# Kernel optimization log

Hardware: AMD Instinct MI355X
Metric: run time of the kernel (lower is better)

## Reference

```python
import jax, jax.numpy as jnp
import numpy as np

B, S, H, R = 32, 1024, 1024, 53
EPS = 1e-12
ATT_EPS = 1e10


def setup_inputs() -> dict:
    key = jax.random.key(0)
    ks = jax.random.split(key, 20)
    sc = 0.02
    n = lambda k, shape: jax.random.normal(k, shape, jnp.float32) * sc
    return {
        "relation": jax.random.randint(ks[0], (B, 1), 0, R),
        "last_hidden_size": jax.random.normal(ks[1], (B, S, H), jnp.float32),
        "sub_head": jax.random.randint(ks[2], (B, 1), 0, S),
        "sub_tail": jax.random.randint(ks[3], (B, 1), 0, S),
        "attention_mask": jax.random.randint(ks[4], (B, S), 0, 2).astype(jnp.int32),
        # learned params
        "rel_emb": n(ks[5], (R, H)),
        "Wrf": n(ks[6], (H, H)), "brf": jnp.zeros((H,), jnp.float32),
        "cln_w": jnp.ones((H,), jnp.float32), "cln_b": jnp.zeros((H,), jnp.float32),
        "Wwd": n(ks[7], (H, 2 * H)), "Wbd": n(ks[8], (H, 2 * H)),
        "Wq": n(ks[9], (H, H)), "bq": jnp.zeros((H,), jnp.float32),
        "Wk": n(ks[10], (H, H)), "bk": jnp.zeros((H,), jnp.float32),
        "Wv": n(ks[11], (H, H)), "bv": jnp.zeros((H,), jnp.float32),
        "Wo": n(ks[12], (1, H)), "bo": jnp.zeros((1,), jnp.float32),
    }


def reference(relation, last_hidden_size, sub_head, sub_tail, attention_mask,
              rel_emb, Wrf, brf, cln_w, cln_b, Wwd, Wbd,
              Wq, bq, Wk, bk, Wv, bv, Wo, bo):
    x = last_hidden_size  # [B,S,H]; dropout is identity at inference
    # relation feature: embedding -> linear -> ReLU6
    rel = jnp.clip(jnp.einsum('boh,gh->bog', rel_emb[relation], Wrf) + brf, 0.0, 6.0)  # [B,1,H]
    # gather subject head/tail token features
    bidx = jnp.arange(x.shape[0])[:, None]
    sub = (x[bidx, sub_head] + x[bidx, sub_tail]) * 0.5  # [B,1,H]
    cond = jnp.concatenate([rel, sub], axis=-1)  # [B,1,2H]
    # conditional layer norm: per-example weight/bias generated from cond
    w = jnp.einsum('boc,gc->bog', cond, Wwd) + cln_w  # [B,1,H]
    b = jnp.einsum('boc,gc->bog', cond, Wbd) + cln_b  # [B,1,H]
    mean = jnp.mean(x, axis=-1, keepdims=True)
    c = x - mean
    var = jnp.mean(c * c, axis=-1, keepdims=True)
    normed = c / jnp.sqrt(var + EPS) * w + b  # [B,S,H]
    # ReLU-activated QKV attention with additive mask bias and residual
    q = jax.nn.relu(jnp.einsum('bsh,gh->bsg', normed, Wq) + bq)
    k = jax.nn.relu(jnp.einsum('bsh,gh->bsg', normed, Wk) + bk)
    v = jax.nn.relu(jnp.einsum('bsh,gh->bsg', normed, Wv) + bv)
    e = jnp.einsum('bsh,bth->bst', q, k)  # [B,S,S]
    m = attention_mask.astype(e.dtype)[:, None, :]  # [B,1,S]
    e = e - ATT_EPS * (1.0 - m)
    a = jax.nn.softmax(e, axis=-1)
    hidden = jnp.einsum('bst,bth->bsh', a, v) + normed  # [B,S,H]
    pred_obj_head = (jnp.einsum('bsh,gh->bsg', hidden, Wo) + bo)[..., 0]  # [B,S]
    return (pred_obj_head, hidden)
```

## Files before the change

### kernel.cpp

```cpp
#include <hip/hip_runtime.h>
#include <hip/hip_bf16.h>

#define NB 32
#define NS 1024
#define NH 1024

typedef short s16x4 __attribute__((ext_vector_type(4)));
typedef short s16x8 __attribute__((ext_vector_type(8)));
typedef float f32x4 __attribute__((ext_vector_type(4)));

typedef __attribute__((address_space(3))) void lds_void;
typedef const __attribute__((address_space(1))) void gmem_void;

__device__ __forceinline__ short f2bf(float f) {
  __hip_bfloat16 h = __float2bfloat16(f);
  return *reinterpret_cast<short*>(&h);
}
__device__ __forceinline__ float bf2f(short s) {
  union { unsigned u; float f; } cv;
  cv.u = ((unsigned)(unsigned short)s) << 16;
  return cv.f;
}

__device__ __forceinline__ float wave_reduce_sum(float v) {
#pragma unroll
  for (int o = 32; o; o >>= 1) v += __shfl_xor(v, o);
  return v;
}
__device__ __forceinline__ float wave_reduce_max(float v) {
#pragma unroll
  for (int o = 32; o; o >>= 1) v = fmaxf(v, __shfl_xor(v, o));
  return v;
}
__device__ __forceinline__ float block_reduce_sum(float v, float* red) {
  v = wave_reduce_sum(v);
  __syncthreads();
  if ((threadIdx.x & 63) == 0) red[threadIdx.x >> 6] = v;
  __syncthreads();
  return red[0] + red[1] + red[2] + red[3];
}
__device__ __forceinline__ float block_reduce_max(float v, float* red) {
  v = wave_reduce_max(v);
  __syncthreads();
  if ((threadIdx.x & 63) == 0) red[threadIdx.x >> 6] = v;
  __syncthreads();
  return fmaxf(fmaxf(red[0], red[1]), fmaxf(red[2], red[3]));
}


#define BAR1 do { __builtin_amdgcn_s_barrier();                              \
                  asm volatile("s_waitcnt lgkmcnt(0)" ::: "memory");         \
                  __builtin_amdgcn_sched_barrier(0); } while (0)
#define BAR2 do { __builtin_amdgcn_s_barrier();                              \
                  asm volatile("" ::: "memory"); } while (0)
#define VW   asm volatile("s_waitcnt vmcnt(4)" ::: "memory")

#define GEMM_PRE()                                                           \
  const int tid  = threadIdx.x;                                              \
  const int lane = tid & 63;                                                 \
  const int w    = tid >> 6;                                                 \
  const int wm   = w >> 2, wn = w & 3;                                       \
  const int fr   = lane & 15, fq = lane >> 4;                                \
           \
  const long tA  = (long)(tid >> 3) * 1024 +                                 \
                   (((tid & 7) ^ ((tid >> 3) & 7)) << 3);                    \
                     \
  const int kc0  = (fq * 8) ^ ((fr & 7) * 8);                                \
  const int kc1  = (fq * 8 + 32) ^ ((fr & 7) * 8);                           \
  const int rdA  = wm * 8192 + fr * 64;                                      \
  const int rdB  = 16384 + (wn >> 1) * 8192 + (wn & 1) * 4096 + fr * 64;     \
  const int wsl  = w * 512;                                                  \
  f32x4 acc[8][4];                                                           \
  s16x8 aF[4][2], bF[2][2][2];                                               \
  _Pragma("unroll") for (int i_ = 0; i_ < 8; ++i_)                           \
    _Pragma("unroll") for (int j_ = 0; j_ < 4; ++j_)                         \
      acc[i_][j_] = (f32x4){0.f, 0.f, 0.f, 0.f};

#define STAGE(d, isB, h, kt)                                                 \
  do {                                                                       \
    const short* _g = ((isB) ? gB + (n0 + (h) * 128) * 1024                  \
                             : gA + (m0 + (h) * 128) * 1024) +               \
                      (long)((kt) & 15) * 64 + tA;                           \
    short* _l = lds + (d) * 32768 + (isB) * 16384 + (h) * 8192 + wsl;        \
    __builtin_amdgcn_global_load_lds((gmem_void*)_g, (lds_void*)_l,          \
                                     16, 0, 0);                              \
    __builtin_amdgcn_global_load_lds((gmem_void*)(_g + 65536),               \
                                     (lds_void*)(_l + 4096), 16, 0, 0);      \
  } while (0)

#define RD_A(d, mq)                                                          \
  _Pragma("unroll") for (int mi = 0; mi < 4; ++mi) {                         \
    aF[mi][0] = *(const s16x8*)(lds + (d) * 32768 + rdA + (mq) * 4096 +      \
                                mi * 1024 + kc0);                            \
    aF[mi][1] = *(const s16x8*)(lds + (d) * 32768 + rdA + (mq) * 4096 +      \
                                mi * 1024 + kc1);                            \
  }
#define RD_B(d, nq)                                                          \
  _Pragma("unroll") for (int ni = 0; ni < 2; ++ni) {                         \
    bF[nq][ni][0] = *(const s16x8*)(lds + (d) * 32768 + rdB + (nq) * 2048 +  \
                                    ni * 1024 + kc0);                        \
    bF[nq][ni][1] = *(const s16x8*)(lds + (d) * 32768 + rdB + (nq) * 2048 +  \
                                    ni * 1024 + kc1);                        \
  }
#define MMA(mq, nq)                                                          \
  do {                                                                       \
    __builtin_amdgcn_s_setprio(1);                                           \
    _Pragma("unroll") for (int kk = 0; kk < 2; ++kk)                         \
      _Pragma("unroll") for (int mi = 0; mi < 4; ++mi)                       \
        _Pragma("unroll") for (int ni = 0; ni < 2; ++ni)                     \
          acc[(mq) * 4 + mi][(nq) * 2 + ni] =                                \
              __builtin_amdgcn_mfma_f32_16x16x32_bf16(                       \
                  aF[mi][kk], bF[nq][ni][kk],                                \
                  acc[(mq) * 4 + mi][(nq) * 2 + ni], 0, 0, 0);               \
    __builtin_amdgcn_s_setprio(0);                                           \
  } while (0)

#define GEMM_MAIN()                                                          \
  GEMM_PRE();                                                                \
  STAGE(0, 1, 0, 0); STAGE(0, 1, 1, 0); STAGE(0, 0, 0, 0); STAGE(0, 0, 1, 0);\
  STAGE(1, 1, 0, 1); STAGE(1, 1, 1, 1);                                      \
  VW; BAR2;                                                                  \
  for (int it = 0; it < 8; ++it) {                                           \
    const int t1 = 2 * it + 1, t2 = 2 * it + 2, t3 = 2 * it + 3;             \
    RD_A(0, 0); RD_B(0, 0); STAGE(1, 0, 0, t1); BAR1; MMA(0, 0); BAR2;       \
    RD_B(0, 1);             STAGE(1, 0, 1, t1); BAR1; MMA(0, 1); BAR2;       \
    RD_A(0, 1);             STAGE(0, 1, 0, t2); BAR1; MMA(1, 1); BAR2;       \
                            STAGE(0, 1, 1, t2); BAR1; MMA(1, 0); VW; BAR2;   \
    RD_A(1, 0); RD_B(1, 0); STAGE(0, 0, 0, t2); BAR1; MMA(0, 0); BAR2;       \
    RD_B(1, 1);             STAGE(0, 0, 1, t2); BAR1; MMA(0, 1); BAR2;       \
    RD_A(1, 1);             STAGE(1, 1, 0, t3); BAR1; MMA(1, 1); BAR2;       \
                            STAGE(1, 1, 1, t3); BAR1; MMA(1, 0); VW; BAR2;   \
  }


__global__ __launch_bounds__(256) void cvtw_kernel(const float* __restrict__ Wq,
    const float* __restrict__ Wk, const float* __restrict__ Wv, short* __restrict__ out) {
  long i = ((long)blockIdx.x * 256 + threadIdx.x) * 4;
  int seg = (int)(i >> 20);
  long off = i & 1048575;
  const float* src = seg == 0 ? Wq : (seg == 1 ? Wk : Wv);
  f32x4 v = *(const f32x4*)(src + off);
  s16x4 o = { f2bf(v[0]), f2bf(v[1]), f2bf(v[2]), f2bf(v[3]) };
  *(s16x4*)(out + i) = o;
}

__global__ __launch_bounds__(256) void cond_kernel(const int* __restrict__ relation,
    const float* __restrict__ x, const int* __restrict__ sub_head,
    const int* __restrict__ sub_tail, const float* __restrict__ rel_emb,
    const float* __restrict__ Wrf, const float* __restrict__ brf, float* __restrict__ cond) {
  const int b = blockIdx.x;
  const int gc = blockIdx.y;
  const int tid = threadIdx.x;
  __shared__ float r[NH];
  const int rid = relation[b];
  for (int h = tid * 4; h < NH; h += 1024)
    *(f32x4*)(r + h) = *(const f32x4*)(rel_emb + (long)rid * NH + h);
  if (gc == 0) {
    const int sh = sub_head[b], st = sub_tail[b];
    for (int h = tid * 4; h < NH; h += 1024) {
      f32x4 a = *(const f32x4*)(x + ((long)b * NS + sh) * NH + h);
      f32x4 c = *(const f32x4*)(x + ((long)b * NS + st) * NH + h);
      f32x4 o = { 0.5f * (a[0] + c[0]), 0.5f * (a[1] + c[1]),
                  0.5f * (a[2] + c[2]), 0.5f * (a[3] + c[3]) };
      *(f32x4*)(cond + b * 2 * NH + NH + h) = o;
    }
  }
  __syncthreads();
  const int lane = tid & 63, wid = tid >> 6;
#pragma unroll
  for (int gi = 0; gi < 16; ++gi) {
    const int g = gc * 64 + wid * 16 + gi;
    float s = 0.f;
#pragma unroll
    for (int h = lane * 4; h < NH; h += 256) {
      f32x4 wv = *(const f32x4*)(Wrf + (long)g * NH + h);
      f32x4 rv = *(const f32x4*)(r + h);
      s += wv[0] * rv[0] + wv[1] * rv[1] + wv[2] * rv[2] + wv[3] * rv[3];
    }
    s = wave_reduce_sum(s);
    if (lane == 0) cond[b * 2 * NH + g] = fminf(fmaxf(s + brf[g], 0.f), 6.f);
  }
}

__global__ __launch_bounds__(256) void wb_kernel(const float* __restrict__ cond,
    const float* __restrict__ Wwd, const float* __restrict__ Wbd,
    const float* __restrict__ cln_w, const float* __restrict__ cln_b,
    float* __restrict__ wln, float* __restrict__ bln) {
  const int g = blockIdx.x;
  const int tid = threadIdx.x;
  __shared__ float wrow[2 * NH];
  __shared__ float brow[2 * NH];
  for (int i = tid * 4; i < 2 * NH; i += 1024) {
    *(f32x4*)(wrow + i) = *(const f32x4*)(Wwd + (long)g * 2 * NH + i);
    *(f32x4*)(brow + i) = *(const f32x4*)(Wbd + (long)g * 2 * NH + i);
  }
  __syncthreads();
  const int lane = tid & 63, wid = tid >> 6;
  const float cw = cln_w[g], cb = cln_b[g];
  for (int b = wid; b < NB; b += 4) {
    float sw = 0.f, sb = 0.f;
#pragma unroll
    for (int c = lane * 4; c < 2 * NH; c += 256) {
      f32x4 cv = *(const f32x4*)(cond + b * 2 * NH + c);
      f32x4 wv = *(const f32x4*)(wrow + c);
      f32x4 bv = *(const f32x4*)(brow + c);
      sw += cv[0] * wv[0] + cv[1] * wv[1] + cv[2] * wv[2] + cv[3] * wv[3];
      sb += cv[0] * bv[0] + cv[1] * bv[1] + cv[2] * bv[2] + cv[3] * bv[3];
    }
    sw = wave_reduce_sum(sw);
    sb = wave_reduce_sum(sb);
    if (lane == 0) {
      wln[b * NH + g] = sw + cw;
      bln[b * NH + g] = sb + cb;
    }
  }
}

__global__ __launch_bounds__(256) void ln_kernel(const float* __restrict__ x,
    const float* __restrict__ wln, const float* __restrict__ bln, short* __restrict__ normed) {
  const long row = blockIdx.x;
  const int tid = threadIdx.x;
  const long b = row >> 10;
  __shared__ float red[4];
  f32x4 v = *(const f32x4*)(x + row * NH + tid * 4);
  float mean = block_reduce_sum(v[0] + v[1] + v[2] + v[3], red) * (1.f / NH);
  float c0 = v[0] - mean, c1 = v[1] - mean, c2 = v[2] - mean, c3 = v[3] - mean;
  float var = block_reduce_sum(c0 * c0 + c1 * c1 + c2 * c2 + c3 * c3, red) * (1.f / NH);
  float rstd = rsqrtf(var + 1e-12f);
  f32x4 wv = *(const f32x4*)(wln + b * NH + tid * 4);
  f32x4 bv = *(const f32x4*)(bln + b * NH + tid * 4);
  s16x4 o = { f2bf(c0 * rstd * wv[0] + bv[0]), f2bf(c1 * rstd * wv[1] + bv[1]),
              f2bf(c2 * rstd * wv[2] + bv[2]), f2bf(c3 * rstd * wv[3] + bv[3]) };
  *(s16x4*)(normed + row * NH + tid * 4) = o;
}

__global__ __launch_bounds__(512, 2) void qkv_kernel(const short* __restrict__ A,
    const short* __restrict__ Wqkv,
    const float* __restrict__ bq, const float* __restrict__ bk, const float* __restrict__ bv,
    short* __restrict__ q, short* __restrict__ k, short* __restrict__ vT) {
  __shared__ short lds[67584];
  const int flat = blockIdx.y * 12 + blockIdx.x;
  const int gid  = (flat & 7) * 192 + (flat >> 3);
  const int mt = gid / 12, nt = gid % 12;
  const short* gA = A;
  const short* gB = Wqkv;
  const long n0 = (long)nt * 256;
  const long m0 = (long)mt * 256;
  GEMM_MAIN();
  const int z = nt >> 2;
  const long hc0 = (long)(nt & 3) * 256;
  const float* bias = z == 0 ? bq : (z == 1 ? bk : bv);
  if (z < 2) {
    short* dst = z == 0 ? q : k;
#pragma unroll
    for (int nI = 0; nI < 4; ++nI) {
      const long col = hc0 + wn * 64 + nI * 16 + fr;
      const float bcol = bias[col];
#pragma unroll
      for (int mI = 0; mI < 8; ++mI)
#pragma unroll
        for (int r = 0; r < 4; ++r) {
          const long row = m0 + wm * 128 + mI * 16 + fq * 4 + r;
          dst[row * NH + col] = f2bf(fmaxf(acc[mI][nI][r] + bcol, 0.f));
        }
    }
  } else {
    asm volatile("s_waitcnt vmcnt(0)" ::: "memory");
    __syncthreads();
#pragma unroll
    for (int nI = 0; nI < 4; ++nI) {
      const int hl = wn * 64 + nI * 16 + fr;
      const float bcol = bias[hc0 + hl];
#pragma unroll
      for (int mI = 0; mI < 8; ++mI) {
        const int tl = wm * 128 + mI * 16 + fq * 4;
        s16x4 pk = { f2bf(fmaxf(acc[mI][nI][0] + bcol, 0.f)),
                     f2bf(fmaxf(acc[mI][nI][1] + bcol, 0.f)),
                     f2bf(fmaxf(acc[mI][nI][2] + bcol, 0.f)),
                     f2bf(fmaxf(acc[mI][nI][3] + bcol, 0.f)) };
        *(s16x4*)(lds + hl * 264 + tl) = pk;
      }
    }
    __syncthreads();
    const int h = tid >> 1, half = tid & 1;
    const long bb = m0 >> 10;
    short* dst = vT + ((bb * NH) + hc0 + h) * NS + (m0 & 1023) + half * 128;
    const short* src = lds + h * 264 + half * 128;
#pragma unroll
    for (int j = 0; j < 16; ++j)
      *(s16x8*)(dst + j * 8) = *(const s16x8*)(src + j * 8);
  }
}

__global__ __launch_bounds__(512, 2) void escore_kernel(const short* __restrict__ q,
    const short* __restrict__ k, const int* __restrict__ amask, float* __restrict__ e) {
  __shared__ short lds[65536];
  const int flat = blockIdx.z * 16 + blockIdx.y * 4 + blockIdx.x;
  const int gid  = (flat & 7) * 64 + (flat >> 3);
  const int b = gid >> 4, mt = (gid >> 2) & 3, nt = gid & 3;
  const short* gA = q + (long)b * NS * NH;
  const short* gB = k + (long)b * NS * NH;
  const long m0 = (long)mt * 256;
  const long n0 = (long)nt * 256;
  GEMM_MAIN();
  float* eb = e + (long)b * NS * NS;
#pragma unroll
  for (int mI = 0; mI < 8; ++mI)
#pragma unroll
    for (int nI = 0; nI < 4; ++nI) {
      const long col = n0 + wn * 64 + nI * 16 + fr;
      const float mb = -1e10f * (1.f - (float)amask[b * NS + col]);
#pragma unroll
      for (int r = 0; r < 4; ++r) {
        const long row = m0 + wm * 128 + mI * 16 + fq * 4 + r;
        eb[row * NS + col] = acc[mI][nI][r] + mb;
      }
    }
}

__global__ __launch_bounds__(256) void softmax_kernel(const float* __restrict__ e,
    short* __restrict__ a, float* __restrict__ inv_sum) {
  const long row = blockIdx.x;
  const int tid = threadIdx.x;
  __shared__ float red[4];
  f32x4 v = *(const f32x4*)(e + row * NS + tid * 4);
  float m = block_reduce_max(fmaxf(fmaxf(v[0], v[1]), fmaxf(v[2], v[3])), red);
  float p0 = expf(v[0] - m), p1 = expf(v[1] - m);
  float p2 = expf(v[2] - m), p3 = expf(v[3] - m);
  float s = block_reduce_sum(p0 + p1 + p2 + p3, red);
  s16x4 o = { f2bf(p0), f2bf(p1), f2bf(p2), f2bf(p3) };
  *(s16x4*)(a + row * NS + tid * 4) = o;
  if (tid == 0) inv_sum[row] = 1.f / s;
}

__global__ __launch_bounds__(512, 2) void av_kernel(const short* __restrict__ a,
    const short* __restrict__ vT, const float* __restrict__ inv_sum,
    const short* __restrict__ normed, const float* __restrict__ Wo,
    float* __restrict__ hid, float* __restrict__ pred_part) {
  __shared__ short lds[65536];
  const int flat = blockIdx.z * 16 + blockIdx.y * 4 + blockIdx.x;
  const int gid  = (flat & 7) * 64 + (flat >> 3);
  const int b = gid >> 4, mt = (gid >> 2) & 3, nt = gid & 3;
  const short* gA = a + (long)b * NS * NS;
  const short* gB = vT + (long)b * NH * NS;
  const long m0 = (long)mt * 256;
  const long n0 = (long)nt * 256;
  GEMM_MAIN();
  float pp[8][4];
#pragma unroll
  for (int mI = 0; mI < 8; ++mI)
#pragma unroll
    for (int r = 0; r < 4; ++r) pp[mI][r] = 0.f;
#pragma unroll
  for (int nI = 0; nI < 4; ++nI) {
    const long col = n0 + wn * 64 + nI * 16 + fr;
    const float wo = Wo[col];
#pragma unroll
    for (int mI = 0; mI < 8; ++mI)
#pragma unroll
      for (int r = 0; r < 4; ++r) {
        const long row = m0 + wm * 128 + mI * 16 + fq * 4 + r;
        const long gi = ((long)b * NS + row) * NH + col;
        float hv = acc[mI][nI][r] * inv_sum[b * NS + row] + bf2f(normed[gi]);
        hid[gi] = hv;
        pp[mI][r] += hv * wo;
      }
  }
#pragma unroll
  for (int mI = 0; mI < 8; ++mI)
#pragma unroll
    for (int r = 0; r < 4; ++r) {
      float v = pp[mI][r];
      v += __shfl_xor(v, 1);
      v += __shfl_xor(v, 2);
      v += __shfl_xor(v, 4);
      v += __shfl_xor(v, 8);
      if (fr == 0)
        pred_part[((long)nt * 4 + wn) * (NB * NS) + (long)b * NS + m0 +
                  wm * 128 + mI * 16 + fq * 4 + r] = v;
    }
}

__global__ __launch_bounds__(256) void pred_finish_kernel(const float* __restrict__ pp,
    const float* __restrict__ bo, float* __restrict__ pred) {
  const int i = (blockIdx.x * 256 + threadIdx.x) * 4;
  const float bz = bo[0];
  f32x4 o = { bz, bz, bz, bz };
#pragma unroll
  for (int j = 0; j < 16; ++j) {
    f32x4 a = *(const f32x4*)(pp + (long)j * (NB * NS) + i);
    o[0] += a[0]; o[1] += a[1]; o[2] += a[2]; o[3] += a[3];
  }
  *(f32x4*)(pred + i) = o;
}

extern "C" void kernel_launch(void* const* d_in, const int* in_sizes, int n_in,
                              void* d_out, int out_size, void* d_ws, size_t ws_size,
                              hipStream_t stream) {
  (void)in_sizes; (void)n_in; (void)out_size; (void)ws_size;
  const int*   relation = (const int*)d_in[0];
  const float* x        = (const float*)d_in[1];
  const int*   sub_head = (const int*)d_in[2];
  const int*   sub_tail = (const int*)d_in[3];
  const int*   amask    = (const int*)d_in[4];
  const float* rel_emb  = (const float*)d_in[5];
  const float* Wrf      = (const float*)d_in[6];
  const float* brf      = (const float*)d_in[7];
  const float* cln_w    = (const float*)d_in[8];
  const float* cln_b    = (const float*)d_in[9];
  const float* Wwd      = (const float*)d_in[10];
  const float* Wbd      = (const float*)d_in[11];
  const float* Wq       = (const float*)d_in[12];
  const float* bq       = (const float*)d_in[13];
  const float* Wk       = (const float*)d_in[14];
  const float* bk       = (const float*)d_in[15];
  const float* Wv       = (const float*)d_in[16];
  const float* bv       = (const float*)d_in[17];
  const float* Wo       = (const float*)d_in[18];
  const float* bo       = (const float*)d_in[19];

  char* ws = (char*)d_ws;
  short* wqkv_bf = (short*)ws;
  float* cond    = (float*)(ws + 6291456);
  float* wln     = cond + 32 * 2048;
  float* bln     = wln + 32 * 1024;
  float* inv_sum = bln + 32 * 1024;
  short* normed  = (short*)(inv_sum + 32768);
  short* qb      = normed + 33554432;
  short* kb      = qb + 33554432;
  short* vT      = kb + 33554432;
  float* e       = (float*)(vT + 33554432);
  float* pred_part = e + 33554432;

  float* pred = (float*)d_out;
  float* hid  = pred + 32768;

  cvtw_kernel<<<3072, 256, 0, stream>>>(Wq, Wk, Wv, wqkv_bf);
  cond_kernel<<<dim3(NB, 16), 256, 0, stream>>>(relation, x, sub_head, sub_tail,
                                                rel_emb, Wrf, brf, cond);
  wb_kernel<<<NH, 256, 0, stream>>>(cond, Wwd, Wbd, cln_w, cln_b, wln, bln);
  ln_kernel<<<NB * NS, 256, 0, stream>>>(x, wln, bln, normed);
  qkv_kernel<<<dim3(12, 128), 512, 0, stream>>>(normed, wqkv_bf,
                                                bq, bk, bv, qb, kb, vT);
  escore_kernel<<<dim3(4, 4, 32), 512, 0, stream>>>(qb, kb, amask, e);
  softmax_kernel<<<NB * NS, 256, 0, stream>>>(e, qb, inv_sum);
  av_kernel<<<dim3(4, 4, 32), 512, 0, stream>>>(qb, vT, inv_sum, normed, Wo,
                                                hid, pred_part);
  pred_finish_kernel<<<32, 256, 0, stream>>>(pred_part, bo, pred);
}
```

Baseline: 534.3 us.

## Replace eight-phase interleaved GEMM schedule with simple double-buffered k-tile loop

Replaces the hand-interleaved main loop, which issued partial global-to-LDS stages between each MMA quarter with barriers around every phase, by a plain double-buffered loop. Each iteration waits for the current k-tile, reads all fragments, runs the four MMA quarters, then prefetches tile t+2 into the freed buffer. This cuts the barrier count per k-tile and lets the compiler overlap LDS reads with MFMAs, at the cost of coarser overlap between global loads and compute. A second A-fragment register set is added, which raises register pressure.

After: 553.1 us. 1.04x slower.

```diff
diff --git a/kernel.cpp b/kernel.cpp
--- a/kernel.cpp
+++ b/kernel.cpp
@@ -47,13 +47,6 @@
   return fmaxf(fmaxf(red[0], red[1]), fmaxf(red[2], red[3]));
 }
 
-
-#define BAR1 do { __builtin_amdgcn_s_barrier();                              \
-                  asm volatile("s_waitcnt lgkmcnt(0)" ::: "memory");         \
-                  __builtin_amdgcn_sched_barrier(0); } while (0)
-#define BAR2 do { __builtin_amdgcn_s_barrier();                              \
-                  asm volatile("" ::: "memory"); } while (0)
-#define VW   asm volatile("s_waitcnt vmcnt(4)" ::: "memory")
 
 #define GEMM_PRE()                                                           \
   const int tid  = threadIdx.x;                                              \
@@ -71,7 +64,7 @@
   const int rdB  = 16384 + (wn >> 1) * 8192 + (wn & 1) * 4096 + fr * 64;     \
   const int wsl  = w * 512;                                                  \
   f32x4 acc[8][4];                                                           \
-  s16x8 aF[4][2], bF[2][2][2];                                               \
+  s16x8 aF[2][4][2], bF[2][2][2];                                            \
   _Pragma("unroll") for (int i_ = 0; i_ < 8; ++i_)                           \
     _Pragma("unroll") for (int j_ = 0; j_ < 4; ++j_)                         \
       acc[i_][j_] = (f32x4){0.f, 0.f, 0.f, 0.f};
@@ -88,12 +81,16 @@
                                      (lds_void*)(_l + 4096), 16, 0, 0);      \
   } while (0)
 
+#define STAGE_T(d, kt)                                                       \
+  do { STAGE(d, 0, 0, kt); STAGE(d, 0, 1, kt);                               \
+       STAGE(d, 1, 0, kt); STAGE(d, 1, 1, kt); } while (0)
+
 #define RD_A(d, mq)                                                          \
   _Pragma("unroll") for (int mi = 0; mi < 4; ++mi) {                         \
-    aF[mi][0] = *(const s16x8*)(lds + (d) * 32768 + rdA + (mq) * 4096 +      \
-                                mi * 1024 + kc0);                            \
-    aF[mi][1] = *(const s16x8*)(lds + (d) * 32768 + rdA + (mq) * 4096 +      \
-                                mi * 1024 + kc1);                            \
+    aF[mq][mi][0] = *(const s16x8*)(lds + (d) * 32768 + rdA + (mq) * 4096 +  \
+                                    mi * 1024 + kc0);                        \
+    aF[mq][mi][1] = *(const s16x8*)(lds + (d) * 32768 + rdA + (mq) * 4096 +  \
+                                    mi * 1024 + kc1);                        \
   }
 #define RD_B(d, nq)                                                          \
   _Pragma("unroll") for (int ni = 0; ni < 2; ++ni) {                         \
@@ -110,26 +107,27 @@
         _Pragma("unroll") for (int ni = 0; ni < 2; ++ni)                     \
           acc[(mq) * 4 + mi][(nq) * 2 + ni] =                                \
               __builtin_amdgcn_mfma_f32_16x16x32_bf16(                       \
-                  aF[mi][kk], bF[nq][ni][kk],                                \
+                  aF[mq][mi][kk], bF[nq][ni][kk],                            \
                   acc[(mq) * 4 + mi][(nq) * 2 + ni], 0, 0, 0);               \
     __builtin_amdgcn_s_setprio(0);                                           \
   } while (0)
 
 #define GEMM_MAIN()                                                          \
   GEMM_PRE();                                                                \
-  STAGE(0, 1, 0, 0); STAGE(0, 1, 1, 0); STAGE(0, 0, 0, 0); STAGE(0, 0, 1, 0);\
-  STAGE(1, 1, 0, 1); STAGE(1, 1, 1, 1);                                      \
-  VW; BAR2;                                                                  \
-  for (int it = 0; it < 8; ++it) {                                           \
-    const int t1 = 2 * it + 1, t2 = 2 * it + 2, t3 = 2 * it + 3;             \
-    RD_A(0, 0); RD_B(0, 0); STAGE(1, 0, 0, t1); BAR1; MMA(0, 0); BAR2;       \
-    RD_B(0, 1);             STAGE(1, 0, 1, t1); BAR1; MMA(0, 1); BAR2;       \
-    RD_A(0, 1);             STAGE(0, 1, 0, t2); BAR1; MMA(1, 1); BAR2;       \
-                            STAGE(0, 1, 1, t2); BAR1; MMA(1, 0); VW; BAR2;   \
-    RD_A(1, 0); RD_B(1, 0); STAGE(0, 0, 0, t2); BAR1; MMA(0, 0); BAR2;       \
-    RD_B(1, 1);             STAGE(0, 0, 1, t2); BAR1; MMA(0, 1); BAR2;       \
-    RD_A(1, 1);             STAGE(1, 1, 0, t3); BAR1; MMA(1, 1); BAR2;       \
-                            STAGE(1, 1, 1, t3); BAR1; MMA(1, 0); VW; BAR2;   \
+  STAGE_T(0, 0); STAGE_T(1, 1);                                              \
+  for (int t = 0; t < 16; ++t) {                                             \
+    const int D = t & 1;                                                     \
+    if (t == 15) asm volatile("s_waitcnt vmcnt(0)" ::: "memory");            \
+    else         asm volatile("s_waitcnt vmcnt(8)" ::: "memory");            \
+    __builtin_amdgcn_s_barrier();                                            \
+    __builtin_amdgcn_sched_barrier(0);                                       \
+    RD_A(D, 0); RD_B(D, 0); RD_B(D, 1);                                      \
+    MMA(0, 0);                                                               \
+    RD_A(D, 1);                                                              \
+    MMA(0, 1); MMA(1, 0); MMA(1, 1);                                         \
+    asm volatile("s_waitcnt lgkmcnt(0)" ::: "memory");                       \
+    __builtin_amdgcn_s_barrier();                                            \
+    if (t < 14) STAGE_T(D, t + 2);                                           \
   }
 
 
@@ -265,7 +263,6 @@
         }
     }
   } else {
-    asm volatile("s_waitcnt vmcnt(0)" ::: "memory");
     __syncthreads();
 #pragma unroll
     for (int nI = 0; nI < 4; ++nI) {
```
